# Performance work log

Measured on AMD Instinct MI355X. Metric: run time of the kernel, lower is better.

## Reference

```python
import jax, jax.numpy as jnp
import numpy as np

TEMP = 0.2
EPS = 1e-12  # F.normalize eps


def setup_inputs() -> dict:
    key = jax.random.key(0)
    k1, k2 = jax.random.split(key)
    l, B, K, D = 4, 64, 32, 128
    emb_i = jax.random.normal(k1, (l, B, K, D), dtype=jnp.float32)
    emb_j = jax.random.normal(k2, (l, B, K, D), dtype=jnp.float32)
    joint_valid = jnp.ones((B, K), dtype=jnp.float32)
    return {"emb_i": emb_i, "emb_j": emb_j, "joint_valid": joint_valid}


def _l2norm(x):
    n = jnp.sqrt(jnp.sum(x * x, axis=-1, keepdims=True))
    return x / jnp.maximum(n, EPS)


def reference(emb_i, emb_j, joint_valid):
    l, B, K, D = emb_i.shape
    N = B * K
    z_i = _l2norm(emb_i.reshape(l, N, D))
    z_j = _l2norm(emb_j.reshape(l, N, D))
    reps = jnp.concatenate([z_i, z_j], axis=1)              # (l, 2N, D), unit rows
    # cosine similarity of unit vectors == matmul
    sim = jnp.einsum('lnd,lmd->lnm', reps, reps)            # (l, 2N, 2N)
    idx = jnp.arange(N)
    pos = sim[:, idx, idx + N]                              # diag offset +N, (l, N)
    # note: original code uses the SAME +N offset diagonal for both ij and ji
    positives = jnp.concatenate([pos, pos], axis=1)         # (l, 2N)
    neg_mask = 1.0 - jnp.eye(2 * N, dtype=sim.dtype)        # (2N, 2N)
    denom = jnp.sum(neg_mask[None] * jnp.exp(sim / TEMP), axis=2)  # (l, 2N)
    loss_partial = -jnp.log(jnp.exp(positives / TEMP) / denom)    # (l, 2N)
    joints_mask = joint_valid.reshape(1, 1, B, K)
    all_num = jnp.sum(joint_valid)
    loss = jnp.sum(loss_partial.reshape(l, 2, B, K) * joints_mask) / (2.0 * all_num)
    return loss
```

## Files before the change

kernel.cpp:

```cpp
#include <hip/hip_runtime.h>
#include <hip/hip_bf16.h>

typedef __attribute__((ext_vector_type(8))) short short8;
typedef __attribute__((ext_vector_type(4))) float floatx4;

#define NROWS 4096
#define NHALF 2048
#define DDIM  128
#define LDST  136
#define SQRT_SCALE 2.6857914f
#define LN2 0.69314718056f

#define WS_ROWSUM_OFF 64
#define WS_DIAG_OFF   16448
#define WS_POS_OFF    32832
#define WS_Z_BYTE_OFF 196864

__device__ inline unsigned short f2bf(float f) {
    unsigned u = __builtin_bit_cast(unsigned, f);
    u += 0x7fffu + ((u >> 16) & 1u);
    return (unsigned short)(u >> 16);
}

__global__ __launch_bounds__(256) void k_norm(const float* __restrict__ emb_i,
                                              const float* __restrict__ emb_j,
                                              const float* __restrict__ jv,
                                              float* __restrict__ wsf,
                                              unsigned short* __restrict__ z) {
    int bx = blockIdx.x, tid = threadIdx.x;
    if (bx == 4096) {
        __shared__ float sred[256];
        float s = 0.f;
        #pragma unroll
        for (int i = 0; i < 8; ++i) s += jv[tid + 256 * i];
        sred[tid] = s; __syncthreads();
        for (int off = 128; off > 0; off >>= 1) {
            if (tid < off) sred[tid] += sred[tid + off];
            __syncthreads();
        }
        if (tid == 0) wsf[1] = sred[0];
        return;
    }
    int gid = bx * 256 + tid;
    if (gid == 0) wsf[0] = 0.f;
    if (gid >= WS_ROWSUM_OFF && gid < WS_ROWSUM_OFF + 16384) wsf[gid] = 0.f;

    int wave = tid >> 6, lane = tid & 63;
    int r = bx * 4 + wave;
    int l = r >> 12, n = r & 4095;
    const float* src = (n < NHALF) ? (emb_i + ((size_t)l * NHALF + n) * DDIM)
                                   : (emb_j + ((size_t)l * NHALF + (n - NHALF)) * DDIM);
    float2 v = *(const float2*)(src + lane * 2);
    float ss = v.x * v.x + v.y * v.y;
    #pragma unroll
    for (int off = 1; off < 64; off <<= 1) ss += __shfl_xor(ss, off);
    float inv = SQRT_SCALE / fmaxf(sqrtf(ss), 1e-12f);
    unsigned pack = ((unsigned)f2bf(v.y * inv) << 16) | (unsigned)f2bf(v.x * inv);
    *(unsigned*)(z + (size_t)r * DDIM + lane * 2) = pack;
}

__global__ __launch_bounds__(256) void k_sim(const unsigned short* __restrict__ z,
                                             float* __restrict__ rowsum,
                                             float* __restrict__ diag,
                                             float* __restrict__ pos) {
    __shared__ __align__(16) unsigned short lds[128 * LDST];
    int bx = blockIdx.x, tid = threadIdx.x;
    int l = bx & 3, rb = (bx >> 2) & 15, cb = bx >> 6;
    int wave = tid >> 6, lane = tid & 63, m = lane & 15, quad = lane >> 4;
    const unsigned short* zl = z + (size_t)l * NROWS * DDIM;
    int l4 = l * NROWS;
    int wr0 = rb * 256 + wave * 64;

    short8 a[4][4];
    #pragma unroll
    for (int rs = 0; rs < 4; ++rs) {
        const unsigned short* p = zl + (size_t)(wr0 + rs * 16 + m) * DDIM + quad * 8;
        #pragma unroll
        for (int kk = 0; kk < 4; ++kk) a[rs][kk] = *(const short8*)(p + kk * 32);
    }
    floatx4 rsum[4];
    #pragma unroll
    for (int rs = 0; rs < 4; ++rs) rsum[rs] = (floatx4){0.f, 0.f, 0.f, 0.f};

    for (int stg = 0; stg < 4; ++stg) {
        int cg0 = cb * 512 + stg * 128;
        __syncthreads();
        #pragma unroll
        for (int i = 0; i < 8; ++i) {
            int chunk = tid + 256 * i;
            int col = chunk >> 4, off = chunk & 15;
            uint4 d = *(const uint4*)(zl + (size_t)(cg0 + col) * DDIM + off * 8);
            *(uint4*)&lds[col * LDST + off * 8] = d;
        }
        __syncthreads();
        #pragma unroll
        for (int cs = 0; cs < 8; ++cs) {
            int ct = cg0 + cs * 16;
            const unsigned short* lp = &lds[(cs * 16 + m) * LDST + quad * 8];
            short8 b0 = *(const short8*)(lp);
            short8 b1 = *(const short8*)(lp + 32);
            short8 b2 = *(const short8*)(lp + 64);
            short8 b3 = *(const short8*)(lp + 96);
            #pragma unroll
            for (int rs = 0; rs < 4; ++rs) {
                floatx4 acc = (floatx4){0.f, 0.f, 0.f, 0.f};
                acc = __builtin_amdgcn_mfma_f32_16x16x32_bf16(a[rs][0], b0, acc, 0, 0, 0);
                acc = __builtin_amdgcn_mfma_f32_16x16x32_bf16(a[rs][1], b1, acc, 0, 0, 0);
                acc = __builtin_amdgcn_mfma_f32_16x16x32_bf16(a[rs][2], b2, acc, 0, 0, 0);
                acc = __builtin_amdgcn_mfma_f32_16x16x32_bf16(a[rs][3], b3, acc, 0, 0, 0);
                int rowbase = wr0 + rs * 16;
                bool isdiag = (ct == rowbase);
                bool ispos  = (ct == (rowbase ^ 2048));
                if (isdiag || ispos) {
                    int c = m - (quad << 2);
                    if (c >= 0 && c < 4) {
                        float v = acc[c];
                        float* dst = isdiag ? &diag[l4 + rowbase + m]
                                            : &pos[l4 + rowbase + m];
                        *dst = v;
                    }
                }
                #pragma unroll
                for (int c = 0; c < 4; ++c)
                    rsum[rs][c] += __builtin_amdgcn_exp2f(acc[c]);
            }
        }
    }
    #pragma unroll
    for (int off = 1; off < 16; off <<= 1)
        #pragma unroll
        for (int rs = 0; rs < 4; ++rs)
            #pragma unroll
            for (int c = 0; c < 4; ++c)
                rsum[rs][c] += __shfl_xor(rsum[rs][c], off);
    if (m == 0) {
        #pragma unroll
        for (int rs = 0; rs < 4; ++rs)
            #pragma unroll
            for (int c = 0; c < 4; ++c) {
                int rg = wr0 + rs * 16 + quad * 4 + c;
                atomicAdd(&rowsum[l4 + rg], rsum[rs][c]);
            }
    }
}

__global__ __launch_bounds__(256) void k_loss(const float* __restrict__ jv,
                                              const float* __restrict__ rowsum,
                                              const float* __restrict__ diag,
                                              const float* __restrict__ pos,
                                              float* __restrict__ wsf) {
    __shared__ float sred[256];
    int tid = threadIdx.x;
    int r = blockIdx.x * 256 + tid;
    int n = r & 4095;
    float denom = rowsum[r] - __builtin_amdgcn_exp2f(diag[r]);
    float contrib = LN2 * (__builtin_amdgcn_logf(denom) - pos[r]);
    float local = contrib * jv[n & (NHALF - 1)];
    sred[tid] = local; __syncthreads();
    for (int off = 128; off > 0; off >>= 1) {
        if (tid < off) sred[tid] += sred[tid + off];
        __syncthreads();
    }
    if (tid == 0) atomicAdd(&wsf[0], sred[0]);
}

__global__ void k_final(const float* __restrict__ wsf, float* __restrict__ out) {
    if (threadIdx.x == 0) out[0] = wsf[0] / (2.f * wsf[1]);
}

extern "C" void kernel_launch(void* const* d_in, const int* in_sizes, int n_in,
                              void* d_out, int out_size, void* d_ws, size_t ws_size,
                              hipStream_t stream) {
    const float* emb_i = (const float*)d_in[0];
    const float* emb_j = (const float*)d_in[1];
    const float* jv    = (const float*)d_in[2];
    float* wsf    = (float*)d_ws;
    float* rowsum = wsf + WS_ROWSUM_OFF;
    float* diag   = wsf + WS_DIAG_OFF;
    float* pos    = wsf + WS_POS_OFF;
    unsigned short* z = (unsigned short*)((char*)d_ws + WS_Z_BYTE_OFF);
    float* out = (float*)d_out;

    k_norm <<<4097, 256, 0, stream>>>(emb_i, emb_j, jv, wsf, z);
    k_sim  <<<512,  256, 0, stream>>>(z, rowsum, diag, pos);
    k_loss <<<64,   256, 0, stream>>>(jv, rowsum, diag, pos, wsf);
    k_final<<<1,    64,  0, stream>>>(wsf, out);
}
```

Measured before the change: 99.49 us.

## Exploit symmetry of similarity matrix with triangular tiling and fuse final kernel

The similarity kernel now visits only upper-triangular 256x256 tile pairs (I<=J), decoding each block's pair index with a triangular-root formula. Off-diagonal tiles also produce column sums that are atomically added to the rowsums of the J rows, which roughly halves the MFMA and exp work. The positive similarity is written for both halves. The separate final kernel is removed: the loss kernel's last block, found through an atomic counter, writes the output. Launch bounds ask for 2 blocks per SM. The costs are extra LDS reductions, more atomics, and uneven tile counts across blocks.

New measurement: 126.7 us. +27.3%, slower.

```diff
diff --git a/kernel.cpp b/kernel.cpp
--- a/kernel.cpp
+++ b/kernel.cpp
@@ -42,7 +42,7 @@
         return;
     }
     int gid = bx * 256 + tid;
-    if (gid == 0) wsf[0] = 0.f;
+    if (gid == 0) { wsf[0] = 0.f; *(unsigned*)&wsf[2] = 0u; }
     if (gid >= WS_ROWSUM_OFF && gid < WS_ROWSUM_OFF + 16384) wsf[gid] = 0.f;
 
     int wave = tid >> 6, lane = tid & 63;
@@ -59,17 +59,21 @@
     *(unsigned*)(z + (size_t)r * DDIM + lane * 2) = pack;
 }
 
-__global__ __launch_bounds__(256) void k_sim(const unsigned short* __restrict__ z,
-                                             float* __restrict__ rowsum,
-                                             float* __restrict__ diag,
-                                             float* __restrict__ pos) {
+__global__ __launch_bounds__(256, 2) void k_sim(const unsigned short* __restrict__ z,
+                                                float* __restrict__ rowsum,
+                                                float* __restrict__ diag,
+                                                float* __restrict__ pos) {
     __shared__ __align__(16) unsigned short lds[128 * LDST];
     int bx = blockIdx.x, tid = threadIdx.x;
-    int l = bx & 3, rb = (bx >> 2) & 15, cb = bx >> 6;
+    int l = bx & 3, idx = bx >> 2;
+    int J = (int)((sqrtf(8.f * (float)idx + 1.f) - 1.f) * 0.5f);
+    while ((J + 1) * (J + 2) / 2 <= idx) ++J;
+    while (J * (J + 1) / 2 > idx) --J;
+    int I = idx - J * (J + 1) / 2;
     int wave = tid >> 6, lane = tid & 63, m = lane & 15, quad = lane >> 4;
     const unsigned short* zl = z + (size_t)l * NROWS * DDIM;
     int l4 = l * NROWS;
-    int wr0 = rb * 256 + wave * 64;
+    int wr0 = I * 256 + wave * 64;
 
     short8 a[4][4];
     #pragma unroll
@@ -81,9 +85,13 @@
     floatx4 rsum[4];
     #pragma unroll
     for (int rs = 0; rs < 4; ++rs) rsum[rs] = (floatx4){0.f, 0.f, 0.f, 0.f};
-
-    for (int stg = 0; stg < 4; ++stg) {
-        int cg0 = cb * 512 + stg * 128;
+    float csum[16];
+    #pragma unroll
+    for (int g = 0; g < 16; ++g) csum[g] = 0.f;
+
+    #pragma unroll
+    for (int stg = 0; stg < 2; ++stg) {
+        int cg0 = J * 256 + stg * 128;
         __syncthreads();
         #pragma unroll
         for (int i = 0; i < 8; ++i) {
@@ -110,19 +118,26 @@
                 acc = __builtin_amdgcn_mfma_f32_16x16x32_bf16(a[rs][3], b3, acc, 0, 0, 0);
                 int rowbase = wr0 + rs * 16;
                 bool isdiag = (ct == rowbase);
-                bool ispos  = (ct == (rowbase ^ 2048));
+                bool ispos  = (ct == rowbase + 2048);
                 if (isdiag || ispos) {
                     int c = m - (quad << 2);
                     if (c >= 0 && c < 4) {
                         float v = acc[c];
-                        float* dst = isdiag ? &diag[l4 + rowbase + m]
-                                            : &pos[l4 + rowbase + m];
-                        *dst = v;
+                        if (isdiag) diag[l4 + rowbase + m] = v;
+                        else {
+                            pos[l4 + rowbase + m] = v;
+                            pos[l4 + rowbase + m + NHALF] = v;
+                        }
                     }
                 }
+                float t = 0.f;
                 #pragma unroll
-                for (int c = 0; c < 4; ++c)
-                    rsum[rs][c] += __builtin_amdgcn_exp2f(acc[c]);
+                for (int c = 0; c < 4; ++c) {
+                    float e = __builtin_amdgcn_exp2f(acc[c]);
+                    rsum[rs][c] += e;
+                    t += e;
+                }
+                csum[stg * 8 + cs] += t;
             }
         }
     }
@@ -142,13 +157,28 @@
                 atomicAdd(&rowsum[l4 + rg], rsum[rs][c]);
             }
     }
+    if (I != J) {
+        __syncthreads();
+        float* cred = (float*)lds;
+        #pragma unroll
+        for (int g = 0; g < 16; ++g) {
+            float v = csum[g];
+            v += __shfl_xor(v, 16);
+            v += __shfl_xor(v, 32);
+            if (quad == 0) cred[wave * 256 + g * 16 + m] = v;
+        }
+        __syncthreads();
+        float s = cred[tid] + cred[tid + 256] + cred[tid + 512] + cred[tid + 768];
+        atomicAdd(&rowsum[l4 + J * 256 + tid], s);
+    }
 }
 
 __global__ __launch_bounds__(256) void k_loss(const float* __restrict__ jv,
                                               const float* __restrict__ rowsum,
                                               const float* __restrict__ diag,
                                               const float* __restrict__ pos,
-                                              float* __restrict__ wsf) {
+                                              float* __restrict__ wsf,
+                                              float* __restrict__ out) {
     __shared__ float sred[256];
     int tid = threadIdx.x;
     int r = blockIdx.x * 256 + tid;
@@ -161,11 +191,15 @@
         if (tid < off) sred[tid] += sred[tid + off];
         __syncthreads();
     }
-    if (tid == 0) atomicAdd(&wsf[0], sred[0]);
-}
-
-__global__ void k_final(const float* __restrict__ wsf, float* __restrict__ out) {
-    if (threadIdx.x == 0) out[0] = wsf[0] / (2.f * wsf[1]);
+    if (tid == 0) {
+        atomicAdd(&wsf[0], sred[0]);
+        __threadfence();
+        unsigned c = atomicAdd((unsigned*)&wsf[2], 1u);
+        if (c == 63) {
+            float tot = atomicAdd(&wsf[0], 0.f);
+            out[0] = tot / (2.f * wsf[1]);
+        }
+    }
 }
 
 extern "C" void kernel_launch(void* const* d_in, const int* in_sizes, int n_in,
@@ -182,7 +216,6 @@
     float* out = (float*)d_out;
 
     k_norm <<<4097, 256, 0, stream>>>(emb_i, emb_j, jv, wsf, z);
-    k_sim  <<<512,  256, 0, stream>>>(z, rowsum, diag, pos);
-    k_loss <<<64,   256, 0, stream>>>(jv, rowsum, diag, pos, wsf);
-    k_final<<<1,    64,  0, stream>>>(wsf, out);
-}
+    k_sim  <<<544,  256, 0, stream>>>(z, rowsum, diag, pos);
+    k_loss <<<64,   256, 0, stream>>>(jv, rowsum, diag, pos, wsf, out);
+}
```
